# Optimization experiments

Measured on AMD Instinct MI355X. Metric: run time of the kernel, lower is better.

## Reference

```python
import jax, jax.numpy as jnp
import numpy as np

LOG_2PI = float(np.log(2.0 * np.pi))


def setup_inputs() -> dict:
    key = jax.random.key(0)
    k1, k2 = jax.random.split(key)
    M, N, D = 8192, 16384, 16
    x_eval = jax.random.normal(k1, (M, D), dtype=jnp.float32)
    x_base = jax.random.normal(k2, (N, D), dtype=jnp.float32)
    # module stores log_bw = log(bw_init); use log(0.2)
    log_bw = jnp.full((1,), np.log(0.2), dtype=jnp.float32)
    return {"x_eval": x_eval, "x_base": x_base, "log_bw": log_bw}


def reference(x_eval, x_base, log_bw):
    N = x_base.shape[0]
    D = x_base.shape[1]
    bw2 = jnp.exp(2.0 * log_bw)  # bw ** 2, shape [1]
    # pairwise squared distances [M, N] via the gemm-based expansion
    sq_e = jnp.sum(x_eval * x_eval, axis=1, keepdims=True)          # [M, 1]
    sq_b = jnp.sum(x_base * x_base, axis=1, keepdims=True).T        # [1, N]
    cross = jnp.einsum('md,nd->mn', x_eval, x_base)                 # [M, N]
    d2 = sq_e + sq_b - 2.0 * cross                                  # [M, N]
    t2 = -0.5 * d2 / bw2                                            # log Gaussian kernel
    t1 = -0.5 * D * LOG_2PI - log_bw                                # scalar-ish [1]
    val = jnp.exp(t1 + t2).sum(axis=1) / N                          # [M]
    return val
```

## Files before the change

### kernel.cpp

```cpp
#include <hip/hip_runtime.h>
#include <math.h>


#define LOG_2PI_F 1.8378770664093453f
#define LOG2E_F   1.4426950408889634f

#define M_PTS 8192
#define N_PTS 16384
#define NCH   64
#define ROWS_PER_CHUNK (N_PTS / NCH)
#define TPC (ROWS_PER_CHUNK / 32)

typedef __attribute__((ext_vector_type(8)))  short bf16x8;
typedef __attribute__((ext_vector_type(16))) float f32x16;

static __device__ __forceinline__ unsigned short f2bf(float x) {
    unsigned u = __float_as_uint(x);
    u += 0x7fffu + ((u >> 16) & 1u);
    return (unsigned short)(u >> 16);
}
static __device__ __forceinline__ float bf2f(unsigned short h) {
    return __uint_as_float(((unsigned)h) << 16);
}
static __device__ __forceinline__ uint4 pack8(const unsigned short* a) {
    uint4 u;
    u.x = (unsigned)a[0] | ((unsigned)a[1] << 16);
    u.y = (unsigned)a[2] | ((unsigned)a[3] << 16);
    u.z = (unsigned)a[4] | ((unsigned)a[5] << 16);
    u.w = (unsigned)a[6] | ((unsigned)a[7] << 16);
    return u;
}

__global__ __launch_bounds__(256) void kde_pack(
        const float* __restrict__ xe, const float* __restrict__ xb,
        const float* __restrict__ log_bw,
        unsigned short* __restrict__ bh, unsigned short* __restrict__ bl,
        unsigned short* __restrict__ bn,
        unsigned short* __restrict__ eh, unsigned short* __restrict__ el,
        unsigned short* __restrict__ en) {
    int r = blockIdx.x * 256 + threadIdx.x;
    if (r >= N_PTS + M_PTS) return;
    const float k2l = __expf(-2.f * log_bw[0]) * LOG2E_F;

    int is_eval = (r >= N_PTS);
    int rr = is_eval ? (r - N_PTS) : r;
    const float* src = is_eval ? xe : xb;
    float dscale = is_eval ? k2l : 1.0f;

    const float4* row = (const float4*)(src + (size_t)rr * 16);
    unsigned short hs[16], ls[16], ns[16];
    float s = 0.f;
#pragma unroll
    for (int k = 0; k < 4; ++k) {
        float4 v = row[k];
        float c[4] = {v.x, v.y, v.z, v.w};
#pragma unroll
        for (int j = 0; j < 4; ++j) {
            s = fmaf(c[j], c[j], s);
            float d = c[j] * dscale;
            unsigned short h = f2bf(d);
            hs[k*4+j] = h;
            ls[k*4+j] = f2bf(d - bf2f(h));
        }
    }
    float cn = -0.5f * s * k2l;
    unsigned short ch = f2bf(cn);
    unsigned short cl = f2bf(cn - bf2f(ch));
#pragma unroll
    for (int i = 0; i < 16; ++i) ns[i] = 0;
    if (is_eval) { ns[0] = 0x3F80; ns[1] = 0x3F80; ns[2] = ch;     ns[3] = cl; }
    else         { ns[0] = ch;     ns[1] = cl;     ns[2] = 0x3F80; ns[3] = 0x3F80; }

    unsigned short* ph = is_eval ? eh : bh;
    unsigned short* pl = is_eval ? el : bl;
    unsigned short* pn = is_eval ? en : bn;
    uint4* dh = (uint4*)(ph + (size_t)rr * 16);
    uint4* dl = (uint4*)(pl + (size_t)rr * 16);
    uint4* dn = (uint4*)(pn + (size_t)rr * 16);
    dh[0] = pack8(hs); dh[1] = pack8(hs + 8);
    dl[0] = pack8(ls); dl[1] = pack8(ls + 8);
    dn[0] = pack8(ns); dn[1] = pack8(ns + 8);
}

__global__ __launch_bounds__(256, 8) void kde_mfma(
        const unsigned short* __restrict__ eh, const unsigned short* __restrict__ el,
        const unsigned short* __restrict__ en,
        const unsigned short* __restrict__ bh, const unsigned short* __restrict__ bl,
        const unsigned short* __restrict__ bn,
        float* __restrict__ part) {
    const int lane = threadIdx.x & 63;
    const int widx = threadIdx.x >> 6;
    const int b = blockIdx.x;
    const int chunk = b >> 6;
    const int etp = (b & 63) * 4 + widx;
    const int col = lane & 31;
    const int kg  = lane >> 5;

    const size_t eoff = ((size_t)etp * 32 + col) * 16 + (size_t)kg * 8;
    const bf16x8 Bh = *(const bf16x8*)(eh + eoff);
    const bf16x8 Bl = *(const bf16x8*)(el + eoff);
    const bf16x8 Bn = *(const bf16x8*)(en + eoff);

    size_t aoff = ((size_t)chunk * ROWS_PER_CHUNK + col) * 16 + (size_t)kg * 8;
    const unsigned short* pah = bh + aoff;
    const unsigned short* pal = bl + aoff;
    const unsigned short* pan = bn + aoff;

    float acc0 = 0.f, acc1 = 0.f;

#pragma unroll
    for (int t = 0; t < TPC; ++t) {
        const bf16x8 Ah = *(const bf16x8*)pah;
        const bf16x8 Al = *(const bf16x8*)pal;
        const bf16x8 An = *(const bf16x8*)pan;
        pah += 32 * 16; pal += 32 * 16; pan += 32 * 16;

        f32x16 C;
#pragma unroll
        for (int r = 0; r < 16; ++r) C[r] = 0.f;
        C = __builtin_amdgcn_mfma_f32_32x32x16_bf16(Ah, Bh, C, 0, 0, 0);
        C = __builtin_amdgcn_mfma_f32_32x32x16_bf16(Ah, Bl, C, 0, 0, 0);
        C = __builtin_amdgcn_mfma_f32_32x32x16_bf16(Al, Bh, C, 0, 0, 0);
        C = __builtin_amdgcn_mfma_f32_32x32x16_bf16(An, Bn, C, 0, 0, 0);

#pragma unroll
        for (int r = 0; r < 16; r += 2) {
            acc0 += __builtin_amdgcn_exp2f(C[r]);
            acc1 += __builtin_amdgcn_exp2f(C[r + 1]);
        }
    }

    float s = acc0 + acc1;
    s += __shfl_xor(s, 32, 64);
    if (lane < 32)
        part[(size_t)chunk * M_PTS + (size_t)etp * 32 + col] = s;
}

__global__ __launch_bounds__(256) void kde_reduce(
        const float* __restrict__ part, const float* __restrict__ log_bw,
        float* __restrict__ out) {
    int m = blockIdx.x * 256 + threadIdx.x;
    if (m >= M_PTS) return;
    float lb = log_bw[0];
    float scale = __expf(-8.f * LOG_2PI_F - lb) / (float)N_PTS;
    float s = 0.f;
#pragma unroll
    for (int c = 0; c < NCH; ++c) s += part[(size_t)c * M_PTS + m];
    out[m] = scale * s;
}

extern "C" void kernel_launch(void* const* d_in, const int* in_sizes, int n_in,
                              void* d_out, int out_size, void* d_ws, size_t ws_size,
                              hipStream_t stream) {
    const float* xe = (const float*)d_in[0];
    const float* xb = (const float*)d_in[1];
    const float* lb = (const float*)d_in[2];
    float* out = (float*)d_out;

    unsigned short* bh = (unsigned short*)d_ws;
    unsigned short* bl = bh + (size_t)N_PTS * 16;
    unsigned short* bn = bl + (size_t)N_PTS * 16;
    unsigned short* eh = bn + (size_t)N_PTS * 16;
    unsigned short* el = eh + (size_t)M_PTS * 16;
    unsigned short* en = el + (size_t)M_PTS * 16;
    float* part = (float*)(en + (size_t)M_PTS * 16);

    kde_pack<<<(N_PTS + M_PTS) / 256, 256, 0, stream>>>(xe, xb, lb,
                                                        bh, bl, bn, eh, el, en);
    kde_mfma<<<4096, 256, 0, stream>>>(eh, el, en, bh, bl, bn, part);
    kde_reduce<<<M_PTS / 256, 256, 0, stream>>>(part, lb, out);
}
```

Measured before the change: 47.68 us.

## Interleave base hi/lo/norm tiles and split norm into three bf16 terms

Packs the base-point hi, lo and norm bf16 rows into one tiled buffer, so each 32-row tile's three operands sit next to each other and can be fetched as one stream. The squared-norm constant is now split into three bf16 pieces instead of two, which makes the norm term more accurate at no extra MFMA cost. The inner loop is no longer unrolled, which may lower register pressure but gives up the chance to prefetch loads across iterations.

```diff
diff --git a/kernel.cpp b/kernel.cpp
--- a/kernel.cpp
+++ b/kernel.cpp
@@ -10,6 +10,8 @@
 #define NCH   64
 #define ROWS_PER_CHUNK (N_PTS / NCH)
 #define TPC (ROWS_PER_CHUNK / 32)
+#define TILE_USH 1536
+#define CHUNK_USH (TPC * TILE_USH)
 
 typedef __attribute__((ext_vector_type(8)))  short bf16x8;
 typedef __attribute__((ext_vector_type(16))) float f32x16;
@@ -34,8 +36,7 @@
 __global__ __launch_bounds__(256) void kde_pack(
         const float* __restrict__ xe, const float* __restrict__ xb,
         const float* __restrict__ log_bw,
-        unsigned short* __restrict__ bh, unsigned short* __restrict__ bl,
-        unsigned short* __restrict__ bn,
+        unsigned short* __restrict__ bint,
         unsigned short* __restrict__ eh, unsigned short* __restrict__ el,
         unsigned short* __restrict__ en) {
     int r = blockIdx.x * 256 + threadIdx.x;
@@ -64,29 +65,43 @@
         }
     }
     float cn = -0.5f * s * k2l;
-    unsigned short ch = f2bf(cn);
-    unsigned short cl = f2bf(cn - bf2f(ch));
+    unsigned short c0 = f2bf(cn);
+    float r1 = cn - bf2f(c0);
+    unsigned short c1 = f2bf(r1);
+    unsigned short c2 = f2bf(r1 - bf2f(c1));
 #pragma unroll
     for (int i = 0; i < 16; ++i) ns[i] = 0;
-    if (is_eval) { ns[0] = 0x3F80; ns[1] = 0x3F80; ns[2] = ch;     ns[3] = cl; }
-    else         { ns[0] = ch;     ns[1] = cl;     ns[2] = 0x3F80; ns[3] = 0x3F80; }
+    if (is_eval) {
+        ns[0] = 0x3F80; ns[1] = 0x3F80; ns[2] = 0x3F80;
+        ns[3] = c0;     ns[4] = c1;     ns[5] = c2;
+    } else {
+        ns[0] = c0;     ns[1] = c1;     ns[2] = c2;
+        ns[3] = 0x3F80; ns[4] = 0x3F80; ns[5] = 0x3F80;
+    }
 
-    unsigned short* ph = is_eval ? eh : bh;
-    unsigned short* pl = is_eval ? el : bl;
-    unsigned short* pn = is_eval ? en : bn;
-    uint4* dh = (uint4*)(ph + (size_t)rr * 16);
-    uint4* dl = (uint4*)(pl + (size_t)rr * 16);
-    uint4* dn = (uint4*)(pn + (size_t)rr * 16);
-    dh[0] = pack8(hs); dh[1] = pack8(hs + 8);
-    dl[0] = pack8(ls); dl[1] = pack8(ls + 8);
-    dn[0] = pack8(ns); dn[1] = pack8(ns + 8);
+    if (is_eval) {
+        uint4* dh = (uint4*)(eh + (size_t)rr * 16);
+        uint4* dl = (uint4*)(el + (size_t)rr * 16);
+        uint4* dn = (uint4*)(en + (size_t)rr * 16);
+        dh[0] = pack8(hs); dh[1] = pack8(hs + 8);
+        dl[0] = pack8(ls); dl[1] = pack8(ls + 8);
+        dn[0] = pack8(ns); dn[1] = pack8(ns + 8);
+    } else {
+        int t = rr >> 5, q = rr & 31;
+        unsigned short* base = bint + (size_t)t * TILE_USH + q * 16;
+        uint4* dh = (uint4*)(base);
+        uint4* dl = (uint4*)(base + 512);
+        uint4* dn = (uint4*)(base + 1024);
+        dh[0] = pack8(hs); dh[1] = pack8(hs + 8);
+        dl[0] = pack8(ls); dl[1] = pack8(ls + 8);
+        dn[0] = pack8(ns); dn[1] = pack8(ns + 8);
+    }
 }
 
 __global__ __launch_bounds__(256, 8) void kde_mfma(
         const unsigned short* __restrict__ eh, const unsigned short* __restrict__ el,
         const unsigned short* __restrict__ en,
-        const unsigned short* __restrict__ bh, const unsigned short* __restrict__ bl,
-        const unsigned short* __restrict__ bn,
+        const unsigned short* __restrict__ bint,
         float* __restrict__ part) {
     const int lane = threadIdx.x & 63;
     const int widx = threadIdx.x >> 6;
@@ -101,19 +116,17 @@
     const bf16x8 Bl = *(const bf16x8*)(el + eoff);
     const bf16x8 Bn = *(const bf16x8*)(en + eoff);
 
-    size_t aoff = ((size_t)chunk * ROWS_PER_CHUNK + col) * 16 + (size_t)kg * 8;
-    const unsigned short* pah = bh + aoff;
-    const unsigned short* pal = bl + aoff;
-    const unsigned short* pan = bn + aoff;
+    const unsigned short* pa =
+        bint + (size_t)chunk * CHUNK_USH + (size_t)col * 16 + (size_t)kg * 8;
 
     float acc0 = 0.f, acc1 = 0.f;
 
-#pragma unroll
+#pragma unroll 1
     for (int t = 0; t < TPC; ++t) {
-        const bf16x8 Ah = *(const bf16x8*)pah;
-        const bf16x8 Al = *(const bf16x8*)pal;
-        const bf16x8 An = *(const bf16x8*)pan;
-        pah += 32 * 16; pal += 32 * 16; pan += 32 * 16;
+        const bf16x8 Ah = *(const bf16x8*)(pa);
+        const bf16x8 Al = *(const bf16x8*)(pa + 512);
+        const bf16x8 An = *(const bf16x8*)(pa + 1024);
+        pa += TILE_USH;
 
         f32x16 C;
 #pragma unroll
@@ -157,16 +170,14 @@
     const float* lb = (const float*)d_in[2];
     float* out = (float*)d_out;
 
-    unsigned short* bh = (unsigned short*)d_ws;
-    unsigned short* bl = bh + (size_t)N_PTS * 16;
-    unsigned short* bn = bl + (size_t)N_PTS * 16;
-    unsigned short* eh = bn + (size_t)N_PTS * 16;
+    unsigned short* bint = (unsigned short*)d_ws;
+    unsigned short* eh = bint + (size_t)(N_PTS / 32) * TILE_USH;
     unsigned short* el = eh + (size_t)M_PTS * 16;
     unsigned short* en = el + (size_t)M_PTS * 16;
     float* part = (float*)(en + (size_t)M_PTS * 16);
 
     kde_pack<<<(N_PTS + M_PTS) / 256, 256, 0, stream>>>(xe, xb, lb,
-                                                        bh, bl, bn, eh, el, en);
-    kde_mfma<<<4096, 256, 0, stream>>>(eh, el, en, bh, bl, bn, part);
+                                                        bint, eh, el, en);
+    kde_mfma<<<4096, 256, 0, stream>>>(eh, el, en, bint, part);
     kde_reduce<<<M_PTS / 256, 256, 0, stream>>>(part, lb, out);
 }
```

Measured after the change: 48.98 us, median of 3. +2.7%, slower.
